# Performance work log

Hardware: AMD Instinct MI355X
Metric: run time of the kernel (lower is better)

## Reference

```python
import jax, jax.numpy as jnp
import numpy as np

N_NODES = 100000
N_EDGES = 1600000
IN_DIM = 160
HID = 128
BN_EPS = 1e-5


def setup_inputs() -> dict:
    key = jax.random.key(0)
    ks = jax.random.split(key, 16)
    d = {}
    d['x'] = jax.random.normal(ks[0], (N_NODES, IN_DIM), dtype=jnp.float32)
    d['edge_index'] = jax.random.randint(ks[1], (2, N_EDGES), 0, N_NODES, dtype=jnp.int64)
    dims = [(IN_DIM, HID), (HID, HID), (HID, HID)]
    for i, (fi, fo) in enumerate(dims):
        s = 1.0 / np.sqrt(fi)
        d[f'wl{i}'] = jax.random.normal(ks[2 + 4 * i], (fi, fo), dtype=jnp.float32) * s
        d[f'wr{i}'] = jax.random.normal(ks[3 + 4 * i], (fi, fo), dtype=jnp.float32) * s
        d[f'bl{i}'] = jnp.zeros((fo,), dtype=jnp.float32)
        d[f'g{i}'] = jnp.ones((fo,), dtype=jnp.float32)
        d[f'be{i}'] = jnp.zeros((fo,), dtype=jnp.float32)
        d[f'rm{i}'] = jax.random.normal(ks[4 + 4 * i], (fo,), dtype=jnp.float32) * 0.1
        d[f'rv{i}'] = jnp.ones((fo,), dtype=jnp.float32)
    d['lin_w'] = jax.random.normal(ks[14], (HID, 1), dtype=jnp.float32) * (1.0 / np.sqrt(HID))
    d['lin_b'] = jnp.zeros((1,), dtype=jnp.float32)
    return d


def _sage_bn_relu(h, src, dst, wl, wr, bl, g, be, rm, rv):
    # mean neighbor aggregation: gather messages at src, scatter-mean to dst
    msg = h[src]                                            # [E, d]
    agg = jax.ops.segment_sum(msg, dst, num_segments=N_NODES)
    cnt = jax.ops.segment_sum(jnp.ones((msg.shape[0],), h.dtype), dst, num_segments=N_NODES)
    mean = agg / jnp.maximum(cnt, 1.0)[:, None]             # nodes w/o in-edges -> 0
    out = mean @ wl + bl + h @ wr                           # SAGEConv (root_weight=True)
    # BatchNorm1d (inference: running stats) + ReLU
    out = (out - rm) * (g * jax.lax.rsqrt(rv + BN_EPS)) + be
    return jax.nn.relu(out)


def reference(x, edge_index,
              wl0, wr0, bl0, g0, be0, rm0, rv0,
              wl1, wr1, bl1, g1, be1, rm1, rv1,
              wl2, wr2, bl2, g2, be2, rm2, rv2,
              lin_w, lin_b):
    src, dst = edge_index[0], edge_index[1]
    h = _sage_bn_relu(x, src, dst, wl0, wr0, bl0, g0, be0, rm0, rv0)
    h = _sage_bn_relu(h, src, dst, wl1, wr1, bl1, g1, be1, rm1, rv1)
    h = _sage_bn_relu(h, src, dst, wl2, wr2, bl2, g2, be2, rm2, rv2)
    return (h @ lin_w + lin_b)[:, 0]                        # [N]
```

## Files before the change

kernel.cpp:

```cpp
#include <hip/hip_runtime.h>

#define N_NODES 100000
#define N_EDGES 1600000
#define IN_DIM 160
#define HID 128
#define BN_EPS 1e-5f

#define M_PAD 100096
#define NBUCK 196
#define BSH 9
#define EPB 8192
#define NHB (NBUCK * NBUCK)
#define NSB 38
#define LPAD 132
#define NSLOT (NBUCK * 512)

typedef unsigned int uint;
typedef unsigned short ushort;
typedef __attribute__((ext_vector_type(8))) short bf16x8;
typedef __attribute__((ext_vector_type(4))) float f32x4;
typedef __attribute__((ext_vector_type(2))) float f32x2;

__device__ __forceinline__ ushort bf16rn(float f) {
    uint u = __float_as_uint(f);
    u += 0x7fffu + ((u >> 16) & 1u);
    return (ushort)(u >> 16);
}
__device__ __forceinline__ float bflo(uint u) { return __uint_as_float(u << 16); }
__device__ __forceinline__ float bfhi(uint u) { return __uint_as_float(u & 0xffff0000u); }


__device__ __forceinline__ void prep_body(int ob, int lane, const float* __restrict__ wl,
                                          const float* __restrict__ wr,
                                          ushort* __restrict__ Bf, int K) {
    int kb = ob >> 4;
    int tt = ob & 15;
    int n = tt * 16 + (lane & 15);
    int k0 = kb * 32 + (lane >> 4) * 8;
    ushort* dst = Bf + ((size_t)(kb * 16 + tt) * 64 + lane) * 8;
#pragma unroll
    for (int e = 0; e < 8; ++e) {
        int k = k0 + e;
        float v = (n < HID) ? wl[k * HID + n] : wr[k * HID + (n - HID)];
        dst[e] = bf16rn(v);
    }
}

#define PREP0_B 20
#define PREP1_B 16
#define INIT_GRID (NBUCK + PREP0_B + 2 * PREP1_B + 2 + 1)

__global__ __launch_bounds__(256) void init_kernel(
    const int* __restrict__ dst, int* __restrict__ ghist,
    const float* __restrict__ wl0, const float* __restrict__ wr0,
    const float* __restrict__ wl1, const float* __restrict__ wr1,
    const float* __restrict__ wl2, const float* __restrict__ wr2,
    ushort* __restrict__ Bf0, ushort* __restrict__ Bf1, ushort* __restrict__ Bf2,
    const float* __restrict__ bl0, const float* __restrict__ g0,
    const float* __restrict__ be0, const float* __restrict__ rm0,
    const float* __restrict__ rv0,
    const float* __restrict__ bl1, const float* __restrict__ g1,
    const float* __restrict__ be1, const float* __restrict__ rm1,
    const float* __restrict__ rv1,
    const float* __restrict__ bl2, const float* __restrict__ g2,
    const float* __restrict__ be2, const float* __restrict__ rm2,
    const float* __restrict__ rv2,
    float* __restrict__ bnscale, float* __restrict__ bnshift,
    ushort* __restrict__ h) {
    __shared__ int hist[NBUCK];
    int b = blockIdx.x, t = threadIdx.x;
    if (b < NBUCK) {
        for (int i = t; i < NBUCK; i += 256) hist[i] = 0;
        __syncthreads();
        int e0 = b * EPB;
        for (int i = 0; i < EPB; i += 256) {
            int e = e0 + i + t;
            if (e < N_EDGES) atomicAdd(&hist[dst[e] >> BSH], 1);
        }
        __syncthreads();
        for (int i = t; i < NBUCK; i += 256) ghist[i * NBUCK + b] = hist[i];
    } else if (b < NBUCK + PREP0_B) {
        int ob = (b - NBUCK) * 4 + (t >> 6);
        prep_body(ob, t & 63, wl0, wr0, Bf0, IN_DIM);
    } else if (b < NBUCK + PREP0_B + PREP1_B) {
        int ob = (b - NBUCK - PREP0_B) * 4 + (t >> 6);
        prep_body(ob, t & 63, wl1, wr1, Bf1, HID);
    } else if (b < NBUCK + PREP0_B + 2 * PREP1_B) {
        int ob = (b - NBUCK - PREP0_B - PREP1_B) * 4 + (t >> 6);
        prep_body(ob, t & 63, wl2, wr2, Bf2, HID);
    } else if (b < NBUCK + PREP0_B + 2 * PREP1_B + 2) {
        int tt = (b - (NBUCK + PREP0_B + 2 * PREP1_B)) * 256 + t;
        if (tt < 3 * HID) {
            int L = tt >> 7, j = tt & 127;
            const float* bl = (L == 0) ? bl0 : (L == 1) ? bl1 : bl2;
            const float* gg = (L == 0) ? g0  : (L == 1) ? g1  : g2;
            const float* be = (L == 0) ? be0 : (L == 1) ? be1 : be2;
            const float* rm = (L == 0) ? rm0 : (L == 1) ? rm1 : rm2;
            const float* rv = (L == 0) ? rv0 : (L == 1) ? rv1 : rv2;
            float s = gg[j] * rsqrtf(rv[j] + BN_EPS);
            bnscale[tt] = s;
            bnshift[tt] = (bl[j] - rm[j]) * s + be[j];
        }
    } else {
        uint* hp = (uint*)(h + (size_t)N_NODES * HID);
        for (int i = t; i < (M_PAD - N_NODES) * HID / 2; i += 256) hp[i] = 0u;
    }
}


__global__ __launch_bounds__(256) void scan1_kernel(const int* __restrict__ ghist,
                                                    int* __restrict__ bsum) {
    __shared__ int wsum[4];
    int b = blockIdx.x, t = threadIdx.x;
    int i4 = b * 256 + t;
    int4 v = (i4 * 4 < NHB) ? ((const int4*)ghist)[i4] : make_int4(0, 0, 0, 0);
    int s = v.x + v.y + v.z + v.w;
#pragma unroll
    for (int off = 32; off; off >>= 1) s += __shfl_down(s, off);
    if ((t & 63) == 0) wsum[t >> 6] = s;
    __syncthreads();
    if (t == 0) bsum[b] = wsum[0] + wsum[1] + wsum[2] + wsum[3];
}

__global__ void scan2_kernel(const int* __restrict__ bsum, int* __restrict__ boff,
                             int* __restrict__ gbb) {
    int lane = threadIdx.x;
    int v = (lane < NSB) ? bsum[lane] : 0;
    int s = v;
#pragma unroll
    for (int off = 1; off <= 32; off <<= 1) {
        int t2 = __shfl_up(s, off);
        if (lane >= off) s += t2;
    }
    if (lane < NSB) boff[lane] = s - v;
    if (lane == 0) gbb[NBUCK] = N_EDGES;
}

__global__ __launch_bounds__(256) void scan3_kernel(int* __restrict__ ghist,
                                                    const int* __restrict__ boff,
                                                    int* __restrict__ gbb) {
    __shared__ int ts[256];
    int b = blockIdx.x, t = threadIdx.x;
    int i4 = b * 256 + t;
    bool ok = (i4 * 4) < NHB;
    int4 v = ok ? ((const int4*)ghist)[i4] : make_int4(0, 0, 0, 0);
    int s = v.x + v.y + v.z + v.w;
    ts[t] = s;
    __syncthreads();
    for (int off = 1; off < 256; off <<= 1) {
        int a = (t >= off) ? ts[t - off] : 0;
        __syncthreads();
        ts[t] += a;
        __syncthreads();
    }
    int excl = boff[b] + ((t > 0) ? ts[t - 1] : 0);
    if (ok) {
        int idx = i4 * 4;
        int4 w;
        w.x = excl;
        w.y = excl + v.x;
        w.z = excl + v.x + v.y;
        w.w = excl + v.x + v.y + v.z;
        ((int4*)ghist)[i4] = w;
        if (idx % NBUCK == 0) gbb[idx / NBUCK] = w.x;
    }
}


__global__ __launch_bounds__(256) void bucket_csr_kernel(const uint* __restrict__ scat,
                                                         const int* __restrict__ gbb,
                                                         int* __restrict__ prow,
                                                         int* __restrict__ deg,
                                                         int* __restrict__ peidx,
                                                         int* __restrict__ perm) {
    __shared__ int cnt[512], fl[512], pref[512];
    __shared__ int ts[256];
    __shared__ int tot_s;
    __shared__ int clsCnt[8], clsFill[8], clsBase[9];
    int b = blockIdx.x, t = threadIdx.x;
    int beg = gbb[b], end = gbb[b + 1];
    int pb = beg + b * 8192;
    cnt[t] = 0; cnt[t + 256] = 0;
    if (t < 8) { clsCnt[t] = 0; clsFill[t] = 0; }
    __syncthreads();
    for (int i = beg + t; i < end; i += 256)
        atomicAdd(&cnt[scat[i] >> 17], 1);
    __syncthreads();
    int c0 = cnt[2 * t], c1 = cnt[2 * t + 1];
    int g0 = b * 512 + 2 * t;
    int cls0 = (c0 == 0) ? 0 : ((c0 + 15) >> 4); if (cls0 > 7) cls0 = 7;
    int cls1 = (c1 == 0) ? 0 : ((c1 + 15) >> 4); if (cls1 > 7) cls1 = 7;
    if (g0 < N_NODES) atomicAdd(&clsCnt[cls0], 1);
    if (g0 + 1 < N_NODES) atomicAdd(&clsCnt[cls1], 1);
    int p0 = (c0 + 15) & ~15, p1 = (c1 + 15) & ~15;
    ts[t] = p0 + p1;
    __syncthreads();
    for (int off = 1; off < 256; off <<= 1) {
        int v = (t >= off) ? ts[t - off] : 0;
        __syncthreads();
        ts[t] += v;
        __syncthreads();
    }
    int ex = (t > 0) ? ts[t - 1] : 0;
    pref[2 * t] = ex;
    pref[2 * t + 1] = ex + p0;
    fl[t] = 0; fl[t + 256] = 0;
    if (t == 255) tot_s = ts[255];
    if (g0 < N_NODES) { prow[g0] = pb + ex; deg[g0] = c0; }
    if (g0 + 1 < N_NODES) { prow[g0 + 1] = pb + ex + p0; deg[g0 + 1] = c1; }
    __syncthreads();
    if (t == 0) {
        int sacc = 0;
#pragma unroll
        for (int i = 0; i < 8; ++i) { clsBase[i] = sacc; sacc += clsCnt[i]; }
        clsBase[8] = sacc;
    }
    __syncthreads();
    if (g0 < N_NODES) {
        int p = atomicAdd(&clsFill[cls0], 1);
        perm[b * 512 + clsBase[cls0] + p] = g0;
    }
    if (g0 + 1 < N_NODES) {
        int p = atomicAdd(&clsFill[cls1], 1);
        perm[b * 512 + clsBase[cls1] + p] = g0 + 1;
    }
    int vt = clsBase[8];
    for (int i = vt + t; i < 512; i += 256) perm[b * 512 + i] = N_NODES;
    int tot = tot_s;
    for (int i = t; i < tot; i += 256) peidx[pb + i] = N_NODES;
    __syncthreads();
    for (int i = beg + t; i < end; i += 256) {
        uint w = scat[i];
        int nl = (int)(w >> 17);
        int lp = atomicAdd(&fl[nl], 1);
        peidx[pb + pref[nl] + lp] = (int)(w & 0x1FFFFu);
    }
}

template <int K, bool AFP32>
__device__ __forceinline__ void gemm_body(int bx, int t, ushort* ldsA,
                                          const void* __restrict__ A_,
                                          const ushort* __restrict__ Bf,
                                          ushort* __restrict__ tl,
                                          ushort* __restrict__ troot) {
    constexpr int CPR = K / 8;
    constexpr int FULLG = CPR & ~7;
    const int m0b = bx * 64;

#pragma unroll
    for (int i = 0; i < (64 * CPR) / 256; ++i) {
        int cidx = i * 256 + t;
        int row = cidx / CPR;
        int j = cidx - row * CPR;
        bf16x8 v;
        if (AFP32) {
            const float* A = (const float*)A_;
            int m = m0b + row;
            float4 f0 = make_float4(0.f, 0.f, 0.f, 0.f), f1 = f0;
            if (m < N_NODES) {
                f0 = *(const float4*)(A + (size_t)m * K + j * 8);
                f1 = *(const float4*)(A + (size_t)m * K + j * 8 + 4);
            }
            v[0] = (short)bf16rn(f0.x); v[1] = (short)bf16rn(f0.y);
            v[2] = (short)bf16rn(f0.z); v[3] = (short)bf16rn(f0.w);
            v[4] = (short)bf16rn(f1.x); v[5] = (short)bf16rn(f1.y);
            v[6] = (short)bf16rn(f1.z); v[7] = (short)bf16rn(f1.w);
        } else {
            const ushort* A = (const ushort*)A_;
            v = *(const bf16x8*)(A + (size_t)(m0b + row) * K + j * 8);
        }
        int swz = (j < FULLG) ? ((j & ~7) | ((j ^ row) & 7))
                              : ((j & ~3) | ((j ^ row) & 3));
        *(bf16x8*)&ldsA[row * K + swz * 8] = v;
    }
    __syncthreads();

    const int lane = t & 63;
    const int wv = t >> 6;
    const int col = lane & 15;
    const int q = lane >> 4;
    const int rh = wv & 1;
    const int ch = wv >> 1;
    const int row0 = rh * 32 + col;
    f32x4 acc0[8], acc1[8];
#pragma unroll
    for (int tt = 0; tt < 8; ++tt) {
        acc0[tt] = (f32x4){0.f, 0.f, 0.f, 0.f};
        acc1[tt] = (f32x4){0.f, 0.f, 0.f, 0.f};
    }

#pragma unroll
    for (int kb = 0; kb < K / 32; ++kb) {
        int jj = kb * 4 + q;
        int swzj = (jj < FULLG) ? ((jj & ~7) | ((jj ^ col) & 7))
                                : ((jj & ~3) | ((jj ^ col) & 3));
        bf16x8 a0 = *(const bf16x8*)&ldsA[row0 * K + swzj * 8];
        bf16x8 a1 = *(const bf16x8*)&ldsA[(row0 + 16) * K + swzj * 8];
        const ushort* bp = Bf + ((size_t)((kb * 16 + ch * 8) * 64) + lane) * 8;
#pragma unroll
        for (int tt = 0; tt < 8; ++tt) {
            bf16x8 bfr = *(const bf16x8*)(bp + (size_t)tt * 64 * 8);
            acc0[tt] = __builtin_amdgcn_mfma_f32_16x16x32_bf16(a0, bfr, acc0[tt], 0, 0, 0);
            acc1[tt] = __builtin_amdgcn_mfma_f32_16x16x32_bf16(a1, bfr, acc1[tt], 0, 0, 0);
        }
    }

    __syncthreads();
    ushort(*rp)[16][LPAD] = (ushort(*)[16][LPAD])ldsA;
    ushort* outp = ch ? troot : tl;
#pragma unroll
    for (int mt = 0; mt < 2; ++mt) {
        const f32x4* ac = mt ? acc1 : acc0;
#pragma unroll
        for (int tt = 0; tt < 8; ++tt)
#pragma unroll
            for (int r = 0; r < 4; ++r)
                rp[wv][q * 4 + r][tt * 16 + col] = bf16rn(ac[tt][r]);
        int mbase = m0b + rh * 32 + mt * 16;
#pragma unroll
        for (int i = 0; i < 4; ++i) {
            int lin = i * 64 + lane;
            int row = lin >> 4;
            int c16 = lin & 15;
            bf16x8 v = *(const bf16x8*)&rp[wv][row][c16 * 8];
            *(bf16x8*)(outp + (size_t)(mbase + row) * HID + c16 * 8) = v;
        }
    }
}

template <int K, bool AFP32>
__global__ __launch_bounds__(256) void gemm_kernel(const void* __restrict__ A_,
                                                   const ushort* __restrict__ Bf,
                                                   ushort* __restrict__ tl,
                                                   ushort* __restrict__ troot) {
    constexpr int LDSE = (64 * K > 4 * 16 * LPAD) ? 64 * K : 4 * 16 * LPAD;
    __shared__ ushort ldsA[LDSE];
    gemm_body<K, AFP32>(blockIdx.x, threadIdx.x, ldsA, A_, Bf, tl, troot);
}

__global__ __launch_bounds__(256) void scatter_gemm1_kernel(
    const int* __restrict__ src, const int* __restrict__ dst,
    const int* __restrict__ ghist, uint* __restrict__ scat,
    const float* __restrict__ x, const ushort* __restrict__ Bf0,
    ushort* __restrict__ tl, ushort* __restrict__ troot) {
    constexpr int LDSE = (64 * IN_DIM > 4 * 16 * LPAD) ? 64 * IN_DIM : 4 * 16 * LPAD;
    __shared__ ushort ldsA[LDSE];
    int b = blockIdx.x, t = threadIdx.x;
    if (b < NBUCK) {
        int* base = (int*)ldsA;
        int* fill = base + NBUCK;
        for (int i = t; i < NBUCK; i += 256) { base[i] = ghist[i * NBUCK + b]; fill[i] = 0; }
        __syncthreads();
        int e0 = b * EPB;
        for (int i = 0; i < EPB; i += 256) {
            int e = e0 + i + t;
            if (e < N_EDGES) {
                int d = dst[e];
                int sv = src[e];
                int bk = d >> BSH;
                int lp = atomicAdd(&fill[bk], 1);
                scat[base[bk] + lp] = (uint)sv | ((uint)(d & 511) << 17);
            }
        }
    } else {
        gemm_body<IN_DIM, true>(b - NBUCK, t, ldsA, x, Bf0, tl, troot);
    }
}

template <bool FINAL>
__global__ __launch_bounds__(256) void agg_kernel(
    const ushort* __restrict__ tl_, const ushort* __restrict__ troot_,
    const int* __restrict__ prow, const int* __restrict__ deg_,
    const int* __restrict__ peidx, const int* __restrict__ perm,
    const float* __restrict__ bnscale, const float* __restrict__ bnshift,
    const float* __restrict__ linw, const float* __restrict__ linb,
    ushort* __restrict__ hout, float* __restrict__ out) {
    const int lane = threadIdx.x & 63;
    const int wvg = (blockIdx.x * 256 + (int)threadIdx.x) >> 6;
    const int g = lane >> 4;
    const int s = lane & 15;
    const int slot = wvg * 4 + g;
    const int n = perm[slot];
    const bool valid = (n < N_NODES);
    const int nn = valid ? n : 0;

    float4 sc0 = *(const float4*)(bnscale + s * 8);
    float4 sc1 = *(const float4*)(bnscale + s * 8 + 4);
    float4 sh0 = *(const float4*)(bnshift + s * 8);
    float4 sh1 = *(const float4*)(bnshift + s * 8 + 4);

    int pbeg = prow[nn];
    int dg = valid ? deg_[nn] : 0;
    int myb = (dg + 15) >> 4;

    f32x2 acc2[4];
#pragma unroll
    for (int i = 0; i < 4; ++i) acc2[i] = (f32x2){0.f, 0.f};

    const int gsel = (lane & 48) << 2;

    bool act = (0 < myb);
    int idx = act ? peidx[pbeg + s] : N_NODES;
    int b = 0;
    while (__any(act)) {
        uint4 u[16];
#pragma unroll
        for (int jj = 0; jj < 16; ++jj) {
            int srcj = __builtin_amdgcn_ds_bpermute(gsel | (jj << 2), idx);
            u[jj] = *(const uint4*)(tl_ + (size_t)srcj * HID + s * 8);
        }
        ++b;
        bool actn = (b < myb);
        int idxn = actn ? peidx[pbeg + b * 16 + s] : N_NODES;
#pragma unroll
        for (int jj = 0; jj < 16; ++jj) {
            acc2[0] += (f32x2){bflo(u[jj].x), bfhi(u[jj].x)};
            acc2[1] += (f32x2){bflo(u[jj].y), bfhi(u[jj].y)};
            acc2[2] += (f32x2){bflo(u[jj].z), bfhi(u[jj].z)};
            acc2[3] += (f32x2){bflo(u[jj].w), bfhi(u[jj].w)};
        }
        act = actn; idx = idxn;
    }

    float inv = 1.0f / (float)((dg > 0) ? dg : 1);
    uint4 rv = *(const uint4*)(troot_ + (size_t)nn * HID + s * 8);
    float o[8];
    o[0] = fmaxf(fmaf(fmaf(acc2[0].x, inv, bflo(rv.x)), sc0.x, sh0.x), 0.f);
    o[1] = fmaxf(fmaf(fmaf(acc2[0].y, inv, bfhi(rv.x)), sc0.y, sh0.y), 0.f);
    o[2] = fmaxf(fmaf(fmaf(acc2[1].x, inv, bflo(rv.y)), sc0.z, sh0.z), 0.f);
    o[3] = fmaxf(fmaf(fmaf(acc2[1].y, inv, bfhi(rv.y)), sc0.w, sh0.w), 0.f);
    o[4] = fmaxf(fmaf(fmaf(acc2[2].x, inv, bflo(rv.z)), sc1.x, sh1.x), 0.f);
    o[5] = fmaxf(fmaf(fmaf(acc2[2].y, inv, bfhi(rv.z)), sc1.y, sh1.y), 0.f);
    o[6] = fmaxf(fmaf(fmaf(acc2[3].x, inv, bflo(rv.w)), sc1.z, sh1.z), 0.f);
    o[7] = fmaxf(fmaf(fmaf(acc2[3].y, inv, bfhi(rv.w)), sc1.w, sh1.w), 0.f);

    if (FINAL) {
        float4 w0 = *(const float4*)(linw + s * 8);
        float4 w1 = *(const float4*)(linw + s * 8 + 4);
        float p = o[0] * w0.x + o[1] * w0.y + o[2] * w0.z + o[3] * w0.w +
                  o[4] * w1.x + o[5] * w1.y + o[6] * w1.z + o[7] * w1.w;
#pragma unroll
        for (int off = 1; off < 16; off <<= 1) p += __shfl_xor(p, off);
        if (s == 0 && valid) out[n] = p + linb[0];
    } else {
        if (valid) {
            uint4 pk;
            pk.x = (uint)bf16rn(o[0]) | ((uint)bf16rn(o[1]) << 16);
            pk.y = (uint)bf16rn(o[2]) | ((uint)bf16rn(o[3]) << 16);
            pk.z = (uint)bf16rn(o[4]) | ((uint)bf16rn(o[5]) << 16);
            pk.w = (uint)bf16rn(o[6]) | ((uint)bf16rn(o[7]) << 16);
            *(uint4*)(hout + (size_t)n * HID + s * 8) = pk;
        }
    }
}


extern "C" void kernel_launch(void* const* d_in, const int* in_sizes, int n_in,
                              void* d_out, int out_size, void* d_ws, size_t ws_size,
                              hipStream_t stream) {
    const float* x    = (const float*)d_in[0];
    const int*   ei   = (const int*)d_in[1];
    const int*   esrc = ei;
    const int*   edst = ei + N_EDGES;
    const float* wl[3]; const float* wr[3]; const float* bl[3];
    const float* g[3];  const float* be[3]; const float* rm[3]; const float* rv[3];
    for (int i = 0; i < 3; ++i) {
        wl[i] = (const float*)d_in[2 + 7 * i];
        wr[i] = (const float*)d_in[3 + 7 * i];
        bl[i] = (const float*)d_in[4 + 7 * i];
        g[i]  = (const float*)d_in[5 + 7 * i];
        be[i] = (const float*)d_in[6 + 7 * i];
        rm[i] = (const float*)d_in[7 + 7 * i];
        rv[i] = (const float*)d_in[8 + 7 * i];
    }
    const float* lin_w = (const float*)d_in[23];
    const float* lin_b = (const float*)d_in[24];
    float* out = (float*)d_out;

    char* ws = (char*)d_ws;
    size_t off = 0;
    auto carve = [&](size_t bytes) -> void* {
        void* p = ws + off;
        off += (bytes + 255) & ~(size_t)255;
        return p;
    };
    int*    prow   = (int*)carve((size_t)(N_NODES + 8) * sizeof(int));
    int*    deg    = (int*)carve((size_t)(N_NODES + 8) * sizeof(int));
    int*    peidx  = (int*)carve((size_t)3210000 * sizeof(int));
    uint*   scat   = (uint*)carve((size_t)N_EDGES * sizeof(uint));
    int*    ghist  = (int*)carve((size_t)(NSB * 1024) * sizeof(int));
    int*    gbb    = (int*)carve((NBUCK + 4) * sizeof(int));
    int*    bsum   = (int*)carve((NSB + 2) * sizeof(int));
    int*    boff   = (int*)carve((NSB + 2) * sizeof(int));
    int*    perm   = (int*)carve((size_t)NSLOT * sizeof(int));
    ushort* tl     = (ushort*)carve((size_t)(M_PAD + 1) * HID * sizeof(ushort));
    ushort* troot  = (ushort*)carve((size_t)M_PAD * HID * sizeof(ushort));
    ushort* h      = (ushort*)carve((size_t)M_PAD * HID * sizeof(ushort));
    ushort* Bf0    = (ushort*)carve(256 * IN_DIM * sizeof(ushort));
    ushort* Bf1    = (ushort*)carve(256 * HID * sizeof(ushort));
    ushort* Bf2    = (ushort*)carve(256 * HID * sizeof(ushort));
    float*  bnsc   = (float*)carve(3 * HID * sizeof(float));
    float*  bnsh   = (float*)carve(3 * HID * sizeof(float));
    (void)ws_size; (void)n_in; (void)in_sizes; (void)out_size;

    const int GEMM_GRID = M_PAD / 64;
    const int AGG_GRID = NSLOT / 16;

    init_kernel<<<INIT_GRID, 256, 0, stream>>>(
        edst, ghist,
        wl[0], wr[0], wl[1], wr[1], wl[2], wr[2], Bf0, Bf1, Bf2,
        bl[0], g[0], be[0], rm[0], rv[0],
        bl[1], g[1], be[1], rm[1], rv[1],
        bl[2], g[2], be[2], rm[2], rv[2],
        bnsc, bnsh, h);
    scan1_kernel<<<NSB, 256, 0, stream>>>(ghist, bsum);
    scan2_kernel<<<1, 64, 0, stream>>>(bsum, boff, gbb);
    scan3_kernel<<<NSB, 256, 0, stream>>>(ghist, boff, gbb);
    scatter_gemm1_kernel<<<NBUCK + GEMM_GRID, 256, 0, stream>>>(
        esrc, edst, ghist, scat, x, Bf0, tl, troot);
    bucket_csr_kernel<<<NBUCK, 256, 0, stream>>>(scat, gbb, prow, deg, peidx, perm);

    agg_kernel<false><<<AGG_GRID, 256, 0, stream>>>(tl, troot, prow, deg, peidx, perm,
                                                    bnsc, bnsh, nullptr, nullptr, h, nullptr);
    gemm_kernel<HID, false><<<GEMM_GRID, 256, 0, stream>>>(h, Bf1, tl, troot);
    agg_kernel<false><<<AGG_GRID, 256, 0, stream>>>(tl, troot, prow, deg, peidx, perm,
                                                    bnsc + HID, bnsh + HID, nullptr, nullptr, h, nullptr);
    gemm_kernel<HID, false><<<GEMM_GRID, 256, 0, stream>>>(h, Bf2, tl, troot);
    agg_kernel<true><<<AGG_GRID, 256, 0, stream>>>(tl, troot, prow, deg, peidx, perm,
                                                   bnsc + 2 * HID, bnsh + 2 * HID,
                                                   lin_w, lin_b, nullptr, out);
}
```

Baseline: 442.7 us.

## Fuse neighbor aggregation with next-layer GEMM and drop degree-class permutation

Aggregation and BN/ReLU for layers 1 and 2 now run inside the GEMM kernel. Each block aggregates its 64 rows into LDS as bf16 and then runs the MFMA projection directly, so the intermediate h buffer is no longer written to and re-read from global memory, and two launches go away. Ping-pong tl/troot buffers replace in-place reuse. The degree-class permutation that load-balanced aggregation waves is removed, so nodes are processed in natural order, which may cause wave imbalance. The fused kernel also loses the occupancy and latency hiding of a standalone gather kernel.

Result: no change. 435.1 us (-1.7%).

```diff
diff --git a/kernel.cpp b/kernel.cpp
--- a/kernel.cpp
+++ b/kernel.cpp
@@ -13,7 +13,6 @@
 #define NHB (NBUCK * NBUCK)
 #define NSB 38
 #define LPAD 132
-#define NSLOT (NBUCK * 512)
 
 typedef unsigned int uint;
 typedef unsigned short ushort;
@@ -48,7 +47,7 @@
 
 #define PREP0_B 20
 #define PREP1_B 16
-#define INIT_GRID (NBUCK + PREP0_B + 2 * PREP1_B + 2 + 1)
+#define INIT_GRID (NBUCK + PREP0_B + 2 * PREP1_B + 2)
 
 __global__ __launch_bounds__(256) void init_kernel(
     const int* __restrict__ dst, int* __restrict__ ghist,
@@ -65,8 +64,7 @@
     const float* __restrict__ bl2, const float* __restrict__ g2,
     const float* __restrict__ be2, const float* __restrict__ rm2,
     const float* __restrict__ rv2,
-    float* __restrict__ bnscale, float* __restrict__ bnshift,
-    ushort* __restrict__ h) {
+    float* __restrict__ bnscale, float* __restrict__ bnshift) {
     __shared__ int hist[NBUCK];
     int b = blockIdx.x, t = threadIdx.x;
     if (b < NBUCK) {
@@ -88,7 +86,7 @@
     } else if (b < NBUCK + PREP0_B + 2 * PREP1_B) {
         int ob = (b - NBUCK - PREP0_B - PREP1_B) * 4 + (t >> 6);
         prep_body(ob, t & 63, wl2, wr2, Bf2, HID);
-    } else if (b < NBUCK + PREP0_B + 2 * PREP1_B + 2) {
+    } else {
         int tt = (b - (NBUCK + PREP0_B + 2 * PREP1_B)) * 256 + t;
         if (tt < 3 * HID) {
             int L = tt >> 7, j = tt & 127;
@@ -101,9 +99,6 @@
             bnscale[tt] = s;
             bnshift[tt] = (bl[j] - rm[j]) * s + be[j];
         }
-    } else {
-        uint* hp = (uint*)(h + (size_t)N_NODES * HID);
-        for (int i = t; i < (M_PAD - N_NODES) * HID / 2; i += 256) hp[i] = 0u;
     }
 }
 
@@ -171,27 +166,19 @@
                                                          const int* __restrict__ gbb,
                                                          int* __restrict__ prow,
                                                          int* __restrict__ deg,
-                                                         int* __restrict__ peidx,
-                                                         int* __restrict__ perm) {
+                                                         int* __restrict__ peidx) {
     __shared__ int cnt[512], fl[512], pref[512];
     __shared__ int ts[256];
     __shared__ int tot_s;
-    __shared__ int clsCnt[8], clsFill[8], clsBase[9];
     int b = blockIdx.x, t = threadIdx.x;
     int beg = gbb[b], end = gbb[b + 1];
     int pb = beg + b * 8192;
     cnt[t] = 0; cnt[t + 256] = 0;
-    if (t < 8) { clsCnt[t] = 0; clsFill[t] = 0; }
     __syncthreads();
     for (int i = beg + t; i < end; i += 256)
         atomicAdd(&cnt[scat[i] >> 17], 1);
     __syncthreads();
     int c0 = cnt[2 * t], c1 = cnt[2 * t + 1];
-    int g0 = b * 512 + 2 * t;
-    int cls0 = (c0 == 0) ? 0 : ((c0 + 15) >> 4); if (cls0 > 7) cls0 = 7;
-    int cls1 = (c1 == 0) ? 0 : ((c1 + 15) >> 4); if (cls1 > 7) cls1 = 7;
-    if (g0 < N_NODES) atomicAdd(&clsCnt[cls0], 1);
-    if (g0 + 1 < N_NODES) atomicAdd(&clsCnt[cls1], 1);
     int p0 = (c0 + 15) & ~15, p1 = (c1 + 15) & ~15;
     ts[t] = p0 + p1;
     __syncthreads();
@@ -206,26 +193,10 @@
     pref[2 * t + 1] = ex + p0;
     fl[t] = 0; fl[t + 256] = 0;
     if (t == 255) tot_s = ts[255];
+    int g0 = b * 512 + 2 * t;
     if (g0 < N_NODES) { prow[g0] = pb + ex; deg[g0] = c0; }
     if (g0 + 1 < N_NODES) { prow[g0 + 1] = pb + ex + p0; deg[g0 + 1] = c1; }
     __syncthreads();
-    if (t == 0) {
-        int sacc = 0;
-#pragma unroll
-        for (int i = 0; i < 8; ++i) { clsBase[i] = sacc; sacc += clsCnt[i]; }
-        clsBase[8] = sacc;
-    }
-    __syncthreads();
-    if (g0 < N_NODES) {
-        int p = atomicAdd(&clsFill[cls0], 1);
-        perm[b * 512 + clsBase[cls0] + p] = g0;
-    }
-    if (g0 + 1 < N_NODES) {
-        int p = atomicAdd(&clsFill[cls1], 1);
-        perm[b * 512 + clsBase[cls1] + p] = g0 + 1;
-    }
-    int vt = clsBase[8];
-    for (int i = vt + t; i < 512; i += 256) perm[b * 512 + i] = N_NODES;
     int tot = tot_s;
     for (int i = t; i < tot; i += 256) peidx[pb + i] = N_NODES;
     __syncthreads();
@@ -326,16 +297,6 @@
             *(bf16x8*)(outp + (size_t)(mbase + row) * HID + c16 * 8) = v;
         }
     }
-}
-
-template <int K, bool AFP32>
-__global__ __launch_bounds__(256) void gemm_kernel(const void* __restrict__ A_,
-                                                   const ushort* __restrict__ Bf,
-                                                   ushort* __restrict__ tl,
-                                                   ushort* __restrict__ troot) {
-    constexpr int LDSE = (64 * K > 4 * 16 * LPAD) ? 64 * K : 4 * 16 * LPAD;
-    __shared__ ushort ldsA[LDSE];
-    gemm_body<K, AFP32>(blockIdx.x, threadIdx.x, ldsA, A_, Bf, tl, troot);
 }
 
 __global__ __launch_bounds__(256) void scatter_gemm1_kernel(
@@ -367,30 +328,149 @@
     }
 }
 
-template <bool FINAL>
-__global__ __launch_bounds__(256) void agg_kernel(
+__global__ __launch_bounds__(256) void fused_agg_gemm_kernel(
+    const ushort* __restrict__ tl_in, const ushort* __restrict__ troot_in,
+    const int* __restrict__ prow, const int* __restrict__ deg_,
+    const int* __restrict__ peidx,
+    const float* __restrict__ bnscale, const float* __restrict__ bnshift,
+    const ushort* __restrict__ Bf,
+    ushort* __restrict__ tl_out, ushort* __restrict__ troot_out) {
+    constexpr int K = HID;
+    constexpr int LDSE = (64 * K > 4 * 16 * LPAD) ? 64 * K : 4 * 16 * LPAD;
+    __shared__ ushort ldsA[LDSE];
+    const int t = threadIdx.x;
+    const int lane = t & 63;
+    const int wv = t >> 6;
+    const int m0b = blockIdx.x * 64;
+    const int g = lane >> 4;
+    const int s = lane & 15;
+    const int gsel = (lane & 48) << 2;
+
+    for (int r = 0; r < 4; ++r) {
+        const int row = wv * 16 + r * 4 + g;
+        const int n = m0b + row;
+        const bool valid = (n < N_NODES);
+        const int nn = valid ? n : 0;
+        int pbeg = prow[nn];
+        int dg = valid ? deg_[nn] : 0;
+        int myb = (dg + 15) >> 4;
+
+        f32x2 acc2[4];
+#pragma unroll
+        for (int i = 0; i < 4; ++i) acc2[i] = (f32x2){0.f, 0.f};
+
+        bool act = (0 < myb);
+        int idx = act ? peidx[pbeg + s] : N_NODES;
+        int b = 0;
+        while (__any(act)) {
+            uint4 u[16];
+#pragma unroll
+            for (int jj = 0; jj < 16; ++jj) {
+                int srcj = __builtin_amdgcn_ds_bpermute(gsel | (jj << 2), idx);
+                u[jj] = *(const uint4*)(tl_in + (size_t)srcj * HID + s * 8);
+            }
+            ++b;
+            bool actn = (b < myb);
+            int idxn = actn ? peidx[pbeg + b * 16 + s] : N_NODES;
+#pragma unroll
+            for (int jj = 0; jj < 16; ++jj) {
+                acc2[0] += (f32x2){bflo(u[jj].x), bfhi(u[jj].x)};
+                acc2[1] += (f32x2){bflo(u[jj].y), bfhi(u[jj].y)};
+                acc2[2] += (f32x2){bflo(u[jj].z), bfhi(u[jj].z)};
+                acc2[3] += (f32x2){bflo(u[jj].w), bfhi(u[jj].w)};
+            }
+            act = actn; idx = idxn;
+        }
+
+        float inv = 1.0f / (float)((dg > 0) ? dg : 1);
+        uint4 rv = *(const uint4*)(troot_in + (size_t)nn * HID + s * 8);
+        float4 sc0 = *(const float4*)(bnscale + s * 8);
+        float4 sc1 = *(const float4*)(bnscale + s * 8 + 4);
+        float4 sh0 = *(const float4*)(bnshift + s * 8);
+        float4 sh1 = *(const float4*)(bnshift + s * 8 + 4);
+        float vm = valid ? 1.0f : 0.0f;
+        float o[8];
+        o[0] = fmaxf(fmaf(fmaf(acc2[0].x, inv, bflo(rv.x)), sc0.x, sh0.x), 0.f) * vm;
+        o[1] = fmaxf(fmaf(fmaf(acc2[0].y, inv, bfhi(rv.x)), sc0.y, sh0.y), 0.f) * vm;
+        o[2] = fmaxf(fmaf(fmaf(acc2[1].x, inv, bflo(rv.y)), sc0.z, sh0.z), 0.f) * vm;
+        o[3] = fmaxf(fmaf(fmaf(acc2[1].y, inv, bfhi(rv.y)), sc0.w, sh0.w), 0.f) * vm;
+        o[4] = fmaxf(fmaf(fmaf(acc2[2].x, inv, bflo(rv.z)), sc1.x, sh1.x), 0.f) * vm;
+        o[5] = fmaxf(fmaf(fmaf(acc2[2].y, inv, bfhi(rv.z)), sc1.y, sh1.y), 0.f) * vm;
+        o[6] = fmaxf(fmaf(fmaf(acc2[3].x, inv, bflo(rv.w)), sc1.z, sh1.z), 0.f) * vm;
+        o[7] = fmaxf(fmaf(fmaf(acc2[3].y, inv, bfhi(rv.w)), sc1.w, sh1.w), 0.f) * vm;
+
+        bf16x8 pk;
+#pragma unroll
+        for (int e = 0; e < 8; ++e) pk[e] = (short)bf16rn(o[e]);
+        int swz = (s & ~7) | ((s ^ row) & 7);
+        *(bf16x8*)&ldsA[row * K + swz * 8] = pk;
+    }
+    __syncthreads();
+
+    const int col = lane & 15;
+    const int q = lane >> 4;
+    const int rh = wv & 1;
+    const int ch = wv >> 1;
+    const int row0 = rh * 32 + col;
+    f32x4 acc0[8], acc1[8];
+#pragma unroll
+    for (int tt = 0; tt < 8; ++tt) {
+        acc0[tt] = (f32x4){0.f, 0.f, 0.f, 0.f};
+        acc1[tt] = (f32x4){0.f, 0.f, 0.f, 0.f};
+    }
+#pragma unroll
+    for (int kb = 0; kb < K / 32; ++kb) {
+        int jj = kb * 4 + q;
+        int swzj = (jj & ~7) | ((jj ^ col) & 7);
+        bf16x8 a0 = *(const bf16x8*)&ldsA[row0 * K + swzj * 8];
+        bf16x8 a1 = *(const bf16x8*)&ldsA[(row0 + 16) * K + swzj * 8];
+        const ushort* bp = Bf + ((size_t)((kb * 16 + ch * 8) * 64) + lane) * 8;
+#pragma unroll
+        for (int tt = 0; tt < 8; ++tt) {
+            bf16x8 bfr = *(const bf16x8*)(bp + (size_t)tt * 64 * 8);
+            acc0[tt] = __builtin_amdgcn_mfma_f32_16x16x32_bf16(a0, bfr, acc0[tt], 0, 0, 0);
+            acc1[tt] = __builtin_amdgcn_mfma_f32_16x16x32_bf16(a1, bfr, acc1[tt], 0, 0, 0);
+        }
+    }
+
+    __syncthreads();
+    ushort(*rp)[16][LPAD] = (ushort(*)[16][LPAD])ldsA;
+    ushort* outp = ch ? troot_out : tl_out;
+#pragma unroll
+    for (int mt = 0; mt < 2; ++mt) {
+        const f32x4* ac = mt ? acc1 : acc0;
+#pragma unroll
+        for (int tt = 0; tt < 8; ++tt)
+#pragma unroll
+            for (int rr = 0; rr < 4; ++rr)
+                rp[wv][q * 4 + rr][tt * 16 + col] = bf16rn(ac[tt][rr]);
+        int mbase = m0b + rh * 32 + mt * 16;
+#pragma unroll
+        for (int i = 0; i < 4; ++i) {
+            int lin = i * 64 + lane;
+            int rowi = lin >> 4;
+            int c16 = lin & 15;
+            bf16x8 v = *(const bf16x8*)&rp[wv][rowi][c16 * 8];
+            *(bf16x8*)(outp + (size_t)(mbase + rowi) * HID + c16 * 8) = v;
+        }
+    }
+}
+
+__global__ __launch_bounds__(256) void agg_final_kernel(
     const ushort* __restrict__ tl_, const ushort* __restrict__ troot_,
     const int* __restrict__ prow, const int* __restrict__ deg_,
-    const int* __restrict__ peidx, const int* __restrict__ perm,
+    const int* __restrict__ peidx,
     const float* __restrict__ bnscale, const float* __restrict__ bnshift,
     const float* __restrict__ linw, const float* __restrict__ linb,
-    ushort* __restrict__ hout, float* __restrict__ out) {
+    float* __restrict__ out) {
     const int lane = threadIdx.x & 63;
     const int wvg = (blockIdx.x * 256 + (int)threadIdx.x) >> 6;
     const int g = lane >> 4;
     const int s = lane & 15;
-    const int slot = wvg * 4 + g;
-    const int n = perm[slot];
-    const bool valid = (n < N_NODES);
-    const int nn = valid ? n : 0;
-
-    float4 sc0 = *(const float4*)(bnscale + s * 8);
-    float4 sc1 = *(const float4*)(bnscale + s * 8 + 4);
-    float4 sh0 = *(const float4*)(bnshift + s * 8);
-    float4 sh1 = *(const float4*)(bnshift + s * 8 + 4);
-
-    int pbeg = prow[nn];
-    int dg = valid ? deg_[nn] : 0;
+    const int n = wvg * 4 + g;
+
+    int pbeg = prow[n];
+    int dg = deg_[n];
     int myb = (dg + 15) >> 4;
 
     f32x2 acc2[4];
@@ -423,7 +503,11 @@
     }
 
     float inv = 1.0f / (float)((dg > 0) ? dg : 1);
-    uint4 rv = *(const uint4*)(troot_ + (size_t)nn * HID + s * 8);
+    uint4 rv = *(const uint4*)(troot_ + (size_t)n * HID + s * 8);
+    float4 sc0 = *(const float4*)(bnscale + s * 8);
+    float4 sc1 = *(const float4*)(bnscale + s * 8 + 4);
+    float4 sh0 = *(const float4*)(bnshift + s * 8);
+    float4 sh1 = *(const float4*)(bnshift + s * 8 + 4);
     float o[8];
     o[0] = fmaxf(fmaf(fmaf(acc2[0].x, inv, bflo(rv.x)), sc0.x, sh0.x), 0.f);
     o[1] = fmaxf(fmaf(fmaf(acc2[0].y, inv, bfhi(rv.x)), sc0.y, sh0.y), 0.f);
@@ -434,24 +518,13 @@
     o[6] = fmaxf(fmaf(fmaf(acc2[3].x, inv, bflo(rv.w)), sc1.z, sh1.z), 0.f);
     o[7] = fmaxf(fmaf(fmaf(acc2[3].y, inv, bfhi(rv.w)), sc1.w, sh1.w), 0.f);
 
-    if (FINAL) {
-        float4 w0 = *(const float4*)(linw + s * 8);
-        float4 w1 = *(const float4*)(linw + s * 8 + 4);
-        float p = o[0] * w0.x + o[1] * w0.y + o[2] * w0.z + o[3] * w0.w +
-                  o[4] * w1.x + o[5] * w1.y + o[6] * w1.z + o[7] * w1.w;
-#pragma unroll
-        for (int off = 1; off < 16; off <<= 1) p += __shfl_xor(p, off);
-        if (s == 0 && valid) out[n] = p + linb[0];
-    } else {
-        if (valid) {
-            uint4 pk;
-            pk.x = (uint)bf16rn(o[0]) | ((uint)bf16rn(o[1]) << 16);
-            pk.y = (uint)bf16rn(o[2]) | ((uint)bf16rn(o[3]) << 16);
-            pk.z = (uint)bf16rn(o[4]) | ((uint)bf16rn(o[5]) << 16);
-            pk.w = (uint)bf16rn(o[6]) | ((uint)bf16rn(o[7]) << 16);
-            *(uint4*)(hout + (size_t)n * HID + s * 8) = pk;
-        }
-    }
+    float4 w0 = *(const float4*)(linw + s * 8);
+    float4 w1 = *(const float4*)(linw + s * 8 + 4);
+    float p = o[0] * w0.x + o[1] * w0.y + o[2] * w0.z + o[3] * w0.w +
+              o[4] * w1.x + o[5] * w1.y + o[6] * w1.z + o[7] * w1.w;
+#pragma unroll
+    for (int off = 1; off < 16; off <<= 1) p += __shfl_xor(p, off);
+    if (s == 0) out[n] = p + linb[0];
 }
 
 
@@ -492,10 +565,10 @@
     int*    gbb    = (int*)carve((NBUCK + 4) * sizeof(int));
     int*    bsum   = (int*)carve((NSB + 2) * sizeof(int));
     int*    boff   = (int*)carve((NSB + 2) * sizeof(int));
-    int*    perm   = (int*)carve((size_t)NSLOT * sizeof(int));
-    ushort* tl     = (ushort*)carve((size_t)(M_PAD + 1) * HID * sizeof(ushort));
-    ushort* troot  = (ushort*)carve((size_t)M_PAD * HID * sizeof(ushort));
-    ushort* h      = (ushort*)carve((size_t)M_PAD * HID * sizeof(ushort));
+    ushort* tl0    = (ushort*)carve((size_t)(M_PAD + 1) * HID * sizeof(ushort));
+    ushort* troot0 = (ushort*)carve((size_t)M_PAD * HID * sizeof(ushort));
+    ushort* tl1    = (ushort*)carve((size_t)(M_PAD + 1) * HID * sizeof(ushort));
+    ushort* troot1 = (ushort*)carve((size_t)M_PAD * HID * sizeof(ushort));
     ushort* Bf0    = (ushort*)carve(256 * IN_DIM * sizeof(ushort));
     ushort* Bf1    = (ushort*)carve(256 * HID * sizeof(ushort));
     ushort* Bf2    = (ushort*)carve(256 * HID * sizeof(ushort));
@@ -504,7 +577,7 @@
     (void)ws_size; (void)n_in; (void)in_sizes; (void)out_size;
 
     const int GEMM_GRID = M_PAD / 64;
-    const int AGG_GRID = NSLOT / 16;
+    const int AGGF_GRID = N_NODES / 16;
 
     init_kernel<<<INIT_GRID, 256, 0, stream>>>(
         edst, ghist,
@@ -512,21 +585,19 @@
         bl[0], g[0], be[0], rm[0], rv[0],
         bl[1], g[1], be[1], rm[1], rv[1],
         bl[2], g[2], be[2], rm[2], rv[2],
-        bnsc, bnsh, h);
+        bnsc, bnsh);
     scan1_kernel<<<NSB, 256, 0, stream>>>(ghist, bsum);
     scan2_kernel<<<1, 64, 0, stream>>>(bsum, boff, gbb);
     scan3_kernel<<<NSB, 256, 0, stream>>>(ghist, boff, gbb);
     scatter_gemm1_kernel<<<NBUCK + GEMM_GRID, 256, 0, stream>>>(
-        esrc, edst, ghist, scat, x, Bf0, tl, troot);
-    bucket_csr_kernel<<<NBUCK, 256, 0, stream>>>(scat, gbb, prow, deg, peidx, perm);
-
-    agg_kernel<false><<<AGG_GRID, 256, 0, stream>>>(tl, troot, prow, deg, peidx, perm,
-                                                    bnsc, bnsh, nullptr, nullptr, h, nullptr);
-    gemm_kernel<HID, false><<<GEMM_GRID, 256, 0, stream>>>(h, Bf1, tl, troot);
-    agg_kernel<false><<<AGG_GRID, 256, 0, stream>>>(tl, troot, prow, deg, peidx, perm,
-                                                    bnsc + HID, bnsh + HID, nullptr, nullptr, h, nullptr);
-    gemm_kernel<HID, false><<<GEMM_GRID, 256, 0, stream>>>(h, Bf2, tl, troot);
-    agg_kernel<true><<<AGG_GRID, 256, 0, stream>>>(tl, troot, prow, deg, peidx, perm,
-                                                   bnsc + 2 * HID, bnsh + 2 * HID,
-                                                   lin_w, lin_b, nullptr, out);
-}
+        esrc, edst, ghist, scat, x, Bf0, tl0, troot0);
+    bucket_csr_kernel<<<NBUCK, 256, 0, stream>>>(scat, gbb, prow, deg, peidx);
+
+    fused_agg_gemm_kernel<<<GEMM_GRID, 256, 0, stream>>>(
+        tl0, troot0, prow, deg, peidx, bnsc, bnsh, Bf1, tl1, troot1);
+    fused_agg_gemm_kernel<<<GEMM_GRID, 256, 0, stream>>>(
+        tl1, troot1, prow, deg, peidx, bnsc + HID, bnsh + HID, Bf2, tl0, troot0);
+    agg_final_kernel<<<AGGF_GRID, 256, 0, stream>>>(
+        tl0, troot0, prow, deg, peidx, bnsc + 2 * HID, bnsh + 2 * HID,
+        lin_w, lin_b, out);
+}
```
